# Optimization experiments

Measured on AMD Instinct MI355X. Metric: run time of the kernel, lower is better.

## Reference

```python
import jax, jax.numpy as jnp
import numpy as np

D_MODEL = 1024
NHEAD = 16
HEAD_DIM = D_MODEL // NHEAD


def setup_inputs() -> dict:
    key = jax.random.key(0)
    ks = jax.random.split(key, 11)
    B, T = 2, 2048
    s = 1.0 / np.sqrt(D_MODEL)
    return {
        "query": jax.random.normal(ks[0], (B, T, D_MODEL), jnp.float32),
        "key": jax.random.normal(ks[1], (B, T, D_MODEL), jnp.float32),
        "value": jax.random.normal(ks[2], (B, T, D_MODEL), jnp.float32),
        "Wq": jax.random.normal(ks[3], (D_MODEL, D_MODEL), jnp.float32) * s,
        "bq": jnp.zeros((D_MODEL,), jnp.float32),
        "Wk": jax.random.normal(ks[4], (D_MODEL, D_MODEL), jnp.float32) * s,
        "bk": jnp.zeros((D_MODEL,), jnp.float32),
        "Wv": jax.random.normal(ks[5], (D_MODEL, D_MODEL), jnp.float32) * s,
        "bv": jnp.zeros((D_MODEL,), jnp.float32),
        "Wo": jax.random.normal(ks[6], (D_MODEL, D_MODEL), jnp.float32) * s,
        "bo": jnp.zeros((D_MODEL,), jnp.float32),
    }


def reference(query, key, value, Wq, bq, Wk, bk, Wv, bv, Wo, bo):
    B, T, _ = query.shape
    scale = HEAD_DIM ** -0.5
    # Linear projections (torch Linear: x @ W.T + b)
    Q = query @ Wq.T + bq
    K = key @ Wk.T + bk
    V = value @ Wv.T + bv
    # [B, H, T, hd]
    Q = Q.reshape(B, T, NHEAD, HEAD_DIM).transpose(0, 2, 1, 3)
    K = K.reshape(B, T, NHEAD, HEAD_DIM).transpose(0, 2, 1, 3)
    V = V.reshape(B, T, NHEAD, HEAD_DIM).transpose(0, 2, 1, 3)
    # Attention scores [B, H, T, T]
    scores = jnp.einsum("bhqd,bhkd->bhqk", Q, K) * scale
    probs = jax.nn.softmax(scores, axis=-1)
    # dropout is identity in eval mode
    out = jnp.einsum("bhqk,bhkd->bhqd", probs, V)
    out = out.transpose(0, 2, 1, 3).reshape(B, T, D_MODEL)
    return out @ Wo.T + bo
```

## Files before the change

### kernel.cpp

```cpp
#include <hip/hip_runtime.h>
#include <stdint.h>

#define LOG2E_OVER_SQRTHD 0.18033688011112042f
#define SM_BIAS 12.0f

typedef unsigned short u16;
typedef _Float16 f16;
typedef __attribute__((ext_vector_type(4))) float f32x4;
typedef __attribute__((ext_vector_type(8))) _Float16 f16x8;

static __device__ __forceinline__ u16 f2h_bits(float f) {
  union { f16 h; u16 u; } v; v.h = (f16)f; return v.u;
}

static __device__ __forceinline__ void g2l16(const void* g, void* l) {
  __builtin_amdgcn_global_load_lds((const __attribute__((address_space(1))) void*)g,
                                   (__attribute__((address_space(3))) void*)l,
                                   16, 0, 0);
}

__global__ __launch_bounds__(256) void pack_all(
    const float* __restrict__ q, const float* __restrict__ k, const float* __restrict__ v,
    const float* __restrict__ wq, const float* __restrict__ wk,
    const float* __restrict__ wv, const float* __restrict__ wo,
    u16* __restrict__ X, u16* __restrict__ W) {
  int flat = blockIdx.x * 256 + threadIdx.x;
  const float* src;
  u16* dst;
  int idx;
  if (flat < 3 * 1048576) {
    int z = flat >> 20;
    idx = flat & 1048575;
    src = (z == 0) ? q : (z == 1) ? k : v;
    dst = X + (size_t)z * 4194304;
  } else {
    int f2 = flat - 3 * 1048576;
    int z = f2 >> 18;
    idx = f2 & 262143;
    src = (z == 0) ? wq : (z == 1) ? wk : (z == 2) ? wv : wo;
    dst = W + (size_t)z * 1048576;
  }
  float4 x = ((const float4*)src)[idx];
  ushort4 o;
  o.x = f2h_bits(x.x); o.y = f2h_bits(x.y); o.z = f2h_bits(x.z); o.w = f2h_bits(x.w);
  *(ushort4*)(dst + (size_t)idx * 4) = o;
}

template <bool OUT_F16>
static __device__ __forceinline__ void gemm_body(
    const u16* __restrict__ A, const u16* __restrict__ W,
    const float* __restrict__ bias, void* __restrict__ C,
    int ldc, bool row_bias, float oscale, int bm, int bn) {
  __shared__ u16 As[2][128 * 32];
  __shared__ u16 Bs[2][128 * 32];
  const int tid = threadIdx.x;
  const int lane = tid & 63;
  const int wave = tid >> 6;
  const int wm = wave >> 1, wn = wave & 1;
  const int quad = lane >> 4, l15 = lane & 15;

  f32x4 acc[4][4] = {};

  const int r0 = tid >> 2;
  const int c0 = (tid & 3) * 8;
  const u16* Ab = A + (size_t)bm * 1024 + (size_t)r0 * 1024 + c0;
  const u16* Wb = W + (size_t)bn * 1024 + (size_t)r0 * 1024 + c0;

  g2l16(Ab, As[0] + tid * 8);
  g2l16(Ab + 64 * 1024, As[0] + (256 + tid) * 8);
  g2l16(Wb, Bs[0] + tid * 8);
  g2l16(Wb + 64 * 1024, Bs[0] + (256 + tid) * 8);
  __syncthreads();

  for (int kt = 0; kt < 32; ++kt) {
    const int p = kt & 1;
    if (kt + 1 < 32) {
      const int kc = (kt + 1) * 32;
      g2l16(Ab + kc, As[p ^ 1] + tid * 8);
      g2l16(Ab + 64 * 1024 + kc, As[p ^ 1] + (256 + tid) * 8);
      g2l16(Wb + kc, Bs[p ^ 1] + tid * 8);
      g2l16(Wb + 64 * 1024 + kc, Bs[p ^ 1] + (256 + tid) * 8);
    }
    f16x8 af[4], bw[4];
#pragma unroll
    for (int mt = 0; mt < 4; ++mt)
      af[mt] = *(const f16x8*)(As[p] + (wm * 64 + mt * 16 + l15) * 32 + quad * 8);
#pragma unroll
    for (int nt = 0; nt < 4; ++nt)
      bw[nt] = *(const f16x8*)(Bs[p] + (wn * 64 + nt * 16 + l15) * 32 + quad * 8);
#pragma unroll
    for (int mt = 0; mt < 4; ++mt)
#pragma unroll
      for (int nt = 0; nt < 4; ++nt)
        acc[mt][nt] = __builtin_amdgcn_mfma_f32_16x16x32_f16(af[mt], bw[nt], acc[mt][nt], 0, 0, 0);
    __syncthreads();
  }

#pragma unroll
  for (int mt = 0; mt < 4; ++mt) {
    const int row = bm + wm * 64 + mt * 16 + quad * 4;
#pragma unroll
    for (int nt = 0; nt < 4; ++nt) {
      const int col = bn + wn * 64 + nt * 16 + l15;
      const float bcol = row_bias ? 0.0f : bias[col];
#pragma unroll
      for (int i = 0; i < 4; ++i) {
        const float bb = row_bias ? bias[row + i] : bcol;
        float val = (acc[mt][nt][i] + bb) * oscale;
        if (OUT_F16)
          ((u16*)C)[(size_t)(row + i) * ldc + col] = f2h_bits(val);
        else
          ((float*)C)[(size_t)(row + i) * ldc + col] = val;
      }
    }
  }
}

__global__ __launch_bounds__(256) void gemm_qkv(const u16* __restrict__ X,
    const u16* __restrict__ Wf, const float* __restrict__ bq,
    const float* __restrict__ bk, const float* __restrict__ bv,
    u16* __restrict__ QK, u16* __restrict__ Vt, float qscale) {
  const int z = blockIdx.z;
  if (z == 0) {
    gemm_body<true>(X, Wf, bq, QK, 1024, false, qscale,
                    blockIdx.x * 128, blockIdx.y * 128);
  } else if (z == 1) {
    gemm_body<true>(X + (size_t)4194304, Wf + (size_t)1048576, bk,
                    QK + (size_t)4194304, 1024, false, 1.0f,
                    blockIdx.x * 128, blockIdx.y * 128);
  } else {
    gemm_body<true>(Wf + (size_t)2 * 1048576, X + (size_t)2 * 4194304, bv,
                    Vt, 4096, true, 1.0f,
                    blockIdx.y * 128, blockIdx.x * 128);
  }
}

__global__ __launch_bounds__(256) void gemm_out(const u16* __restrict__ O,
    const u16* __restrict__ Wo, const float* __restrict__ bo,
    float* __restrict__ out) {
  gemm_body<false>(O, Wo, bo, out, 1024, false, 1.0f,
                   blockIdx.x * 128, blockIdx.y * 128);
}

__global__ __launch_bounds__(256) void attn_kernel(const u16* __restrict__ QK,
                                                   const u16* __restrict__ Vt,
                                                   u16* __restrict__ O) {
  constexpr int LSP = 68;
  __shared__ u16 Qs[64 * 64];
  __shared__ u16 Ks[2][64 * 64];
  __shared__ u16 Vts[2][64 * 64];
  __shared__ u16 Ps[4][16 * LSP];

  const u16* Qb = QK;
  const u16* Kb = QK + (size_t)4096 * 1024;

  const int tid = threadIdx.x, lane = tid & 63, wave = tid >> 6;
  const int quad = lane >> 4, l15 = lane & 15;
  const int qt = blockIdx.x, h = blockIdx.y, b = blockIdx.z;
  const size_t qrow0 = (size_t)b * 2048 + qt * 64;
  const size_t kv0 = (size_t)b * 2048;
  const int hc = h * 64;

  const int r0 = tid >> 3;
  const int p0 = tid & 7;
  const int s0 = (p0 ^ (r0 & 7)) * 8;

  const u16* Kbase = Kb + (kv0 + r0) * 1024 + hc + s0;
  const u16* Vbase = Vt + (size_t)(hc + r0) * 4096 + kv0 + s0;

  g2l16(Qb + (qrow0 + r0) * 1024 + hc + s0, Qs + tid * 8);
  g2l16(Qb + (qrow0 + 32 + r0) * 1024 + hc + s0, Qs + (256 + tid) * 8);
  g2l16(Kbase, Ks[0] + tid * 8);
  g2l16(Kbase + 32 * 1024, Ks[0] + (256 + tid) * 8);
  g2l16(Vbase, Vts[0] + tid * 8);
  g2l16(Vbase + (size_t)32 * 4096, Vts[0] + (256 + tid) * 8);
  __syncthreads();

  const int Rq = wave * 16 + l15;
  const f16x8 aq0 = *(const f16x8*)(Qs + Rq * 64 + ((quad ^ (Rq & 7)) * 8));
  const f16x8 aq1 = *(const f16x8*)(Qs + Rq * 64 + (((quad + 4) ^ (Rq & 7)) * 8));

  f32x4 o_acc[4] = {};
  float l_part[4] = {0.f, 0.f, 0.f, 0.f};
  u16* Pw = Ps[wave];

  for (int kt = 0; kt < 32; ++kt) {
    const int p = kt & 1;
    if (kt + 1 < 32) {
      const u16* Kn = Kbase + (size_t)(kt + 1) * 64 * 1024;
      const u16* Vn = Vbase + (size_t)(kt + 1) * 64;
      g2l16(Kn, Ks[p ^ 1] + tid * 8);
      g2l16(Kn + 32 * 1024, Ks[p ^ 1] + (256 + tid) * 8);
      g2l16(Vn, Vts[p ^ 1] + tid * 8);
      g2l16(Vn + (size_t)32 * 4096, Vts[p ^ 1] + (256 + tid) * 8);
    }

    f32x4 s[4];
#pragma unroll
    for (int nt = 0; nt < 4; ++nt)
      s[nt] = f32x4{-SM_BIAS, -SM_BIAS, -SM_BIAS, -SM_BIAS};
#pragma unroll
    for (int nt = 0; nt < 4; ++nt) {
      const int Rk = nt * 16 + l15;
      f16x8 bk0 = *(const f16x8*)(Ks[p] + Rk * 64 + ((quad ^ (Rk & 7)) * 8));
      f16x8 bk1 = *(const f16x8*)(Ks[p] + Rk * 64 + (((quad + 4) ^ (Rk & 7)) * 8));
      s[nt] = __builtin_amdgcn_mfma_f32_16x16x32_f16(aq0, bk0, s[nt], 0, 0, 0);
      s[nt] = __builtin_amdgcn_mfma_f32_16x16x32_f16(aq1, bk1, s[nt], 0, 0, 0);
    }

#pragma unroll
    for (int nt = 0; nt < 4; ++nt)
#pragma unroll
      for (int i = 0; i < 4; ++i) {
        float pe = __builtin_amdgcn_exp2f(s[nt][i]);
        l_part[i] += pe;
        Pw[(quad * 4 + i) * LSP + nt * 16 + l15] = f2h_bits(pe);
      }
    asm volatile("s_waitcnt lgkmcnt(0)" ::: "memory");

    union { f16x8 v; struct { uint2 lo, hi; } h; } ap0, ap1;
    ap0.h.lo = *(const uint2*)(Pw + l15 * LSP + quad * 8);
    ap0.h.hi = *(const uint2*)(Pw + l15 * LSP + quad * 8 + 4);
    ap1.h.lo = *(const uint2*)(Pw + l15 * LSP + 32 + quad * 8);
    ap1.h.hi = *(const uint2*)(Pw + l15 * LSP + 32 + quad * 8 + 4);
#pragma unroll
    for (int ct = 0; ct < 4; ++ct) {
      const int Rv = ct * 16 + l15;
      f16x8 bv0 = *(const f16x8*)(Vts[p] + Rv * 64 + ((quad ^ (Rv & 7)) * 8));
      f16x8 bv1 = *(const f16x8*)(Vts[p] + Rv * 64 + (((quad + 4) ^ (Rv & 7)) * 8));
      o_acc[ct] = __builtin_amdgcn_mfma_f32_16x16x32_f16(ap0.v, bv0, o_acc[ct], 0, 0, 0);
      o_acc[ct] = __builtin_amdgcn_mfma_f32_16x16x32_f16(ap1.v, bv1, o_acc[ct], 0, 0, 0);
    }

    __syncthreads();
  }

#pragma unroll
  for (int i = 0; i < 4; ++i)
#pragma unroll
    for (int d = 1; d < 16; d <<= 1) l_part[i] += __shfl_xor(l_part[i], d);

#pragma unroll
  for (int i = 0; i < 4; ++i) {
    const float inv = 1.0f / l_part[i];
    const size_t row = qrow0 + wave * 16 + quad * 4 + i;
#pragma unroll
    for (int ct = 0; ct < 4; ++ct) {
      float ov = o_acc[ct][i] * inv;
      int col = hc + ct * 16 + l15;
      O[row * 1024 + col] = f2h_bits(ov);
    }
  }
}

extern "C" void kernel_launch(void* const* d_in, const int* in_sizes, int n_in,
                              void* d_out, int out_size, void* d_ws, size_t ws_size,
                              hipStream_t stream) {
  const float* query = (const float*)d_in[0];
  const float* key   = (const float*)d_in[1];
  const float* value = (const float*)d_in[2];
  const float* Wq = (const float*)d_in[3];
  const float* bq = (const float*)d_in[4];
  const float* Wk = (const float*)d_in[5];
  const float* bk = (const float*)d_in[6];
  const float* Wv = (const float*)d_in[7];
  const float* bv = (const float*)d_in[8];
  const float* Wo = (const float*)d_in[9];
  const float* bo = (const float*)d_in[10];
  float* out = (float*)d_out;

  u16* X  = (u16*)d_ws;
  u16* W  = X + (size_t)3 * 4194304;
  u16* QK = W + (size_t)4 * 1048576;
  u16* Vt = QK + (size_t)2 * 4194304;
  u16* O  = X;

  pack_all<<<dim3(16384, 1, 1), 256, 0, stream>>>(query, key, value, Wq, Wk, Wv, Wo, X, W);
  gemm_qkv<<<dim3(32, 8, 3), 256, 0, stream>>>(X, W, bq, bk, bv, QK, Vt,
                                               LOG2E_OVER_SQRTHD);
  attn_kernel<<<dim3(32, 16, 2), 256, 0, stream>>>(QK, Vt, O);
  gemm_out<<<dim3(32, 8, 1), 256, 0, stream>>>(O, W + (size_t)3 * 1048576, bo, out);
}
```

Baseline: 265.4 us.

## Remap attention blocks per XCD and drop K/V double buffering

The attention grid is flattened to 1D and block ids are remapped so every block for a given (batch, head) lands on the same XCD (id & 7), so K/V tiles for that head are shared in that XCD's L2. At the same time the double-buffered K/V LDS tiles become single buffers: each iteration does sync, load, sync with no prefetch overlap. This cuts LDS use, which may allow more resident blocks, but exposes global load latency on every tile.

```diff
diff --git a/kernel.cpp b/kernel.cpp
--- a/kernel.cpp
+++ b/kernel.cpp
@@ -147,8 +147,8 @@
                                                    u16* __restrict__ O) {
   constexpr int LSP = 68;
   __shared__ u16 Qs[64 * 64];
-  __shared__ u16 Ks[2][64 * 64];
-  __shared__ u16 Vts[2][64 * 64];
+  __shared__ u16 Ks[64 * 64];
+  __shared__ u16 Vts[64 * 64];
   __shared__ u16 Ps[4][16 * LSP];
 
   const u16* Qb = QK;
@@ -156,7 +156,14 @@
 
   const int tid = threadIdx.x, lane = tid & 63, wave = tid >> 6;
   const int quad = lane >> 4, l15 = lane & 15;
-  const int qt = blockIdx.x, h = blockIdx.y, b = blockIdx.z;
+
+  const int id = blockIdx.x;
+  const int xcd = id & 7;
+  const int j = id >> 3;
+  const int qt = j & 31;
+  const int hb = xcd + 8 * (j >> 5);
+  const int h = hb & 15, b = hb >> 4;
+
   const size_t qrow0 = (size_t)b * 2048 + qt * 64;
   const size_t kv0 = (size_t)b * 2048;
   const int hc = h * 64;
@@ -165,15 +172,8 @@
   const int p0 = tid & 7;
   const int s0 = (p0 ^ (r0 & 7)) * 8;
 
-  const u16* Kbase = Kb + (kv0 + r0) * 1024 + hc + s0;
-  const u16* Vbase = Vt + (size_t)(hc + r0) * 4096 + kv0 + s0;
-
   g2l16(Qb + (qrow0 + r0) * 1024 + hc + s0, Qs + tid * 8);
   g2l16(Qb + (qrow0 + 32 + r0) * 1024 + hc + s0, Qs + (256 + tid) * 8);
-  g2l16(Kbase, Ks[0] + tid * 8);
-  g2l16(Kbase + 32 * 1024, Ks[0] + (256 + tid) * 8);
-  g2l16(Vbase, Vts[0] + tid * 8);
-  g2l16(Vbase + (size_t)32 * 4096, Vts[0] + (256 + tid) * 8);
   __syncthreads();
 
   const int Rq = wave * 16 + l15;
@@ -185,15 +185,13 @@
   u16* Pw = Ps[wave];
 
   for (int kt = 0; kt < 32; ++kt) {
-    const int p = kt & 1;
-    if (kt + 1 < 32) {
-      const u16* Kn = Kbase + (size_t)(kt + 1) * 64 * 1024;
-      const u16* Vn = Vbase + (size_t)(kt + 1) * 64;
-      g2l16(Kn, Ks[p ^ 1] + tid * 8);
-      g2l16(Kn + 32 * 1024, Ks[p ^ 1] + (256 + tid) * 8);
-      g2l16(Vn, Vts[p ^ 1] + tid * 8);
-      g2l16(Vn + (size_t)32 * 4096, Vts[p ^ 1] + (256 + tid) * 8);
-    }
+    const size_t kr0 = kv0 + (size_t)kt * 64;
+    __syncthreads();
+    g2l16(Kb + (kr0 + r0) * 1024 + hc + s0, Ks + tid * 8);
+    g2l16(Kb + (kr0 + 32 + r0) * 1024 + hc + s0, Ks + (256 + tid) * 8);
+    g2l16(Vt + (size_t)(hc + r0) * 4096 + kr0 + s0, Vts + tid * 8);
+    g2l16(Vt + (size_t)(hc + 32 + r0) * 4096 + kr0 + s0, Vts + (256 + tid) * 8);
+    __syncthreads();
 
     f32x4 s[4];
 #pragma unroll
@@ -202,8 +200,8 @@
 #pragma unroll
     for (int nt = 0; nt < 4; ++nt) {
       const int Rk = nt * 16 + l15;
-      f16x8 bk0 = *(const f16x8*)(Ks[p] + Rk * 64 + ((quad ^ (Rk & 7)) * 8));
-      f16x8 bk1 = *(const f16x8*)(Ks[p] + Rk * 64 + (((quad + 4) ^ (Rk & 7)) * 8));
+      f16x8 bk0 = *(const f16x8*)(Ks + Rk * 64 + ((quad ^ (Rk & 7)) * 8));
+      f16x8 bk1 = *(const f16x8*)(Ks + Rk * 64 + (((quad + 4) ^ (Rk & 7)) * 8));
       s[nt] = __builtin_amdgcn_mfma_f32_16x16x32_f16(aq0, bk0, s[nt], 0, 0, 0);
       s[nt] = __builtin_amdgcn_mfma_f32_16x16x32_f16(aq1, bk1, s[nt], 0, 0, 0);
     }
@@ -226,13 +224,11 @@
 #pragma unroll
     for (int ct = 0; ct < 4; ++ct) {
       const int Rv = ct * 16 + l15;
-      f16x8 bv0 = *(const f16x8*)(Vts[p] + Rv * 64 + ((quad ^ (Rv & 7)) * 8));
-      f16x8 bv1 = *(const f16x8*)(Vts[p] + Rv * 64 + (((quad + 4) ^ (Rv & 7)) * 8));
+      f16x8 bv0 = *(const f16x8*)(Vts + Rv * 64 + ((quad ^ (Rv & 7)) * 8));
+      f16x8 bv1 = *(const f16x8*)(Vts + Rv * 64 + (((quad + 4) ^ (Rv & 7)) * 8));
       o_acc[ct] = __builtin_amdgcn_mfma_f32_16x16x32_f16(ap0.v, bv0, o_acc[ct], 0, 0, 0);
       o_acc[ct] = __builtin_amdgcn_mfma_f32_16x16x32_f16(ap1.v, bv1, o_acc[ct], 0, 0, 0);
     }
-
-    __syncthreads();
   }
 
 #pragma unroll
@@ -278,6 +274,6 @@
   pack_all<<<dim3(16384, 1, 1), 256, 0, stream>>>(query, key, value, Wq, Wk, Wv, Wo, X, W);
   gemm_qkv<<<dim3(32, 8, 3), 256, 0, stream>>>(X, W, bq, bk, bv, QK, Vt,
                                                LOG2E_OVER_SQRTHD);
-  attn_kernel<<<dim3(32, 16, 2), 256, 0, stream>>>(QK, Vt, O);
+  attn_kernel<<<dim3(1024, 1, 1), 256, 0, stream>>>(QK, Vt, O);
   gemm_out<<<dim3(32, 8, 1), 256, 0, stream>>>(O, W + (size_t)3 * 1048576, bo, out);
 }
```

Result: faster. 243.0 us (-8.4%).
